# Performance work log

Hardware: AMD Instinct MI355X
Metric: run time of the kernel (lower is better)

## Reference

```python
import jax, jax.numpy as jnp
import numpy as np

NUM_EMBEDDINGS = 1024
EMBEDDING_DIM = 256


def setup_inputs() -> dict:
    key = jax.random.key(0)
    k_in, k_w = jax.random.split(key)
    inputs = jax.random.normal(k_in, (32, EMBEDDING_DIM, 2048), dtype=jnp.float32)
    # nn.Embedding weight initialized uniform in [-1/K, 1/K]
    bound = 1.0 / NUM_EMBEDDINGS
    weight = jax.random.uniform(k_w, (NUM_EMBEDDINGS, EMBEDDING_DIM),
                                dtype=jnp.float32, minval=-bound, maxval=bound)
    return {"inputs": inputs, "weight": weight}


def reference(inputs, weight):
    B, D, T = inputs.shape
    # [B, D, T] -> [B*T, D]
    flat = jnp.transpose(inputs, (0, 2, 1)).reshape(-1, D)
    distances = (jnp.sum(flat * flat, axis=1, keepdims=True)
                 + jnp.sum(weight * weight, axis=1)
                 - 2.0 * flat @ weight.T)  # [N, K]
    encoding_indices = jnp.argmin(distances, axis=1)  # [N]
    # one-hot @ weight is just a gather
    quantized = weight[encoding_indices].reshape(B, T, D)  # [B, T, D]
    quantized = jnp.transpose(quantized, (0, 2, 1))  # [B, D, T]
    # straight-through estimator
    quantized = inputs + jax.lax.stop_gradient(quantized - inputs)
    return quantized, encoding_indices[:, None]
```

## Files before the change

### kernel.cpp

```cpp
#include <hip/hip_runtime.h>


#define VQ_B   32
#define VQ_D   256
#define VQ_T   2048
#define VQ_K   1024

typedef _Float16 f16x8 __attribute__((ext_vector_type(8)));
typedef _Float16 f16x4 __attribute__((ext_vector_type(4)));
typedef float    f32x4 __attribute__((ext_vector_type(4)));

__global__ __launch_bounds__(256) void vq_wprep_kernel(
    const float* __restrict__ w, float* __restrict__ wnorm,
    _Float16* __restrict__ Wh, _Float16* __restrict__ Wl)
{
    __shared__ double ws_[16][16];
    const int tid = threadIdx.x;
    const int kk  = tid >> 4;
    const int dg  = tid & 15;
    const int k   = blockIdx.x * 16 + kk;
    const float* src = w + (size_t)k * VQ_D + dg * 16;
    double s = 0.0;
    #pragma unroll
    for (int q = 0; q < 4; ++q) {
        float4 v = *(const float4*)(src + q * 4);
        s += (double)v.x * v.x + (double)v.y * v.y
           + (double)v.z * v.z + (double)v.w * v.w;
        const float e4[4] = {v.x, v.y, v.z, v.w};
        f16x4 hv, lv;
        #pragma unroll
        for (int j = 0; j < 4; ++j) {
            const float es = e4[j] * 1024.0f;
            const _Float16 h = (_Float16)es;
            hv[j] = h;
            lv[j] = (_Float16)((es - (float)h) * 16777216.0f);
        }
        *(f16x4*)(Wh + (size_t)k * VQ_D + dg * 16 + q * 4) = hv;
        *(f16x4*)(Wl + (size_t)k * VQ_D + dg * 16 + q * 4) = lv;
    }
    ws_[kk][dg] = s;
    __syncthreads();
    if (dg == 0) {
        double acc = 0.0;
        #pragma unroll
        for (int g = 0; g < 16; ++g) acc += ws_[kk][g];
        wnorm[k] = (float)acc;
    }
}

__global__ __launch_bounds__(256, 2) void vq_mfma_kernel(
    const _Float16* __restrict__ Wh, const _Float16* __restrict__ Wl,
    const float* __restrict__ inp,
    const float* __restrict__ wnorm,
    const float* __restrict__ w,
    float* __restrict__ outq, float* __restrict__ outi)
{
    __shared__ alignas(16) char lds[81920];
    char* Xh = lds;
    char* Xl = lds + 32768;
    char* Wb = lds + 65536;

    const int tid  = threadIdx.x;
    const int lane = tid & 63;
    const int wv   = tid >> 6;
    const int m16  = lane & 15;
    const int quad = lane >> 4;
    const int wm   = wv & 1;
    const int wn   = wv >> 1;
    const int b    = blockIdx.x >> 5;
    const int tt0  = (blockIdx.x & 31) * 64;
    const long bt  = (long)b * VQ_T + tt0;

    const int sel  = tid >> 7;
    const int r128 = tid & 127;
    const _Float16* wsrc = (sel ? Wl : Wh) + (size_t)r128 * VQ_D;
    char* wdst = Wb + (sel * 8 + (r128 >> 6) * 4 + ((r128 >> 4) & 3)) * 1024
               + (r128 & 15) * 16;

    f16x8 wreg[4];
    #pragma unroll
    for (int q = 0; q < 4; ++q)
        wreg[q] = *(const f16x8*)(wsrc + q * 8);

    const int xt = m16 + wv * 16;
    double xacc = 0.0;
    {
        float xv[2][8];
        const float* xp0 = inp + ((size_t)b * VQ_D + quad * 8) * VQ_T + tt0 + xt;
        #pragma unroll
        for (int j = 0; j < 8; ++j)
            xv[0][j] = xp0[(size_t)j * VQ_T];
        #pragma unroll
        for (int c = 0; c < 8; ++c) {
            if (c < 7) {
                const float* xpn = inp
                    + ((size_t)b * VQ_D + (c + 1) * 32 + quad * 8) * VQ_T
                    + tt0 + xt;
                #pragma unroll
                for (int j = 0; j < 8; ++j)
                    xv[(c + 1) & 1][j] = xpn[(size_t)j * VQ_T];
            }
            f16x8 hv, lv;
            #pragma unroll
            for (int j = 0; j < 8; ++j) {
                const float x = xv[c & 1][j];
                xacc += (double)x * (double)x;
                const _Float16 h = (_Float16)x;
                hv[j] = h;
                lv[j] = (_Float16)((x - (float)h) * 16777216.0f);
            }
            const int off = ((c * 4 + quad) * 64 + xt) * 16;
            *(f16x8*)(Xh + off) = hv;
            *(f16x8*)(Xl + off) = lv;
        }
    }
    xacc += __shfl_xor(xacc, 16, 64);
    xacc += __shfl_xor(xacc, 32, 64);
    {
        float* xns = (float*)Wb;
        if (quad == 0) xns[xt] = (float)xacc;
    }
    __syncthreads();
    float xnr[2];
    #pragma unroll
    for (int f = 0; f < 2; ++f)
        xnr[f] = ((const float*)Wb)[wn * 32 + f * 16 + m16];
    __syncthreads();

    float bestv[2] = {3.0e38f, 3.0e38f};
    int   besti[2] = {0, 0};
    f32x4 acch[4][2], accl[4][2];

    for (int s = 0; s < 64; ++s) {
        const int c = s & 7;
        #pragma unroll
        for (int q = 0; q < 4; ++q)
            *(f16x8*)(wdst + q * 256) = wreg[q];
        __syncthreads();
        if (s < 63) {
            const int s1  = s + 1;
            const _Float16* src = wsrc
                + (size_t)((s1 >> 3) * 128) * VQ_D + (s1 & 7) * 32;
            #pragma unroll
            for (int q = 0; q < 4; ++q)
                wreg[q] = *(const f16x8*)(src + q * 8);
        }

        if (c == 0) {
            #pragma unroll
            for (int fm = 0; fm < 4; ++fm)
                #pragma unroll
                for (int fn = 0; fn < 2; ++fn) {
                    acch[fm][fn] = (f32x4){0.f, 0.f, 0.f, 0.f};
                    accl[fm][fn] = (f32x4){0.f, 0.f, 0.f, 0.f};
                }
        }

        f16x8 ah[4], al[4], bh[2], bl[2];
        #pragma unroll
        for (int fm = 0; fm < 4; ++fm) {
            ah[fm] = *(const f16x8*)(Wb + (wm * 4 + fm) * 1024 + lane * 16);
            al[fm] = *(const f16x8*)(Wb + (8 + wm * 4 + fm) * 1024 + lane * 16);
        }
        #pragma unroll
        for (int f = 0; f < 2; ++f) {
            const int off = ((c * 4 + quad) * 64 + wn * 32 + f * 16 + m16) * 16;
            bh[f] = *(const f16x8*)(Xh + off);
            bl[f] = *(const f16x8*)(Xl + off);
        }
        #pragma unroll
        for (int fm = 0; fm < 4; ++fm)
            #pragma unroll
            for (int fn = 0; fn < 2; ++fn) {
                acch[fm][fn] = __builtin_amdgcn_mfma_f32_16x16x32_f16(
                    ah[fm], bh[fn], acch[fm][fn], 0, 0, 0);
                accl[fm][fn] = __builtin_amdgcn_mfma_f32_16x16x32_f16(
                    ah[fm], bl[fn], accl[fm][fn], 0, 0, 0);
                accl[fm][fn] = __builtin_amdgcn_mfma_f32_16x16x32_f16(
                    al[fm], bh[fn], accl[fm][fn], 0, 0, 0);
            }

        if (c == 7) {
            const int k0 = (s >> 3) * 128;
            #pragma unroll
            for (int fm = 0; fm < 4; ++fm) {
                #pragma unroll
                for (int r = 0; r < 4; ++r) {
                    const int kg = k0 + wm * 64 + fm * 16 + quad * 4 + r;
                    const float wnk = wnorm[kg];
                    #pragma unroll
                    for (int fn = 0; fn < 2; ++fn) {
                        const float t1 = xnr[fn] + wnk;
                        const float d2 = (acch[fm][fn][r]
                                          + accl[fm][fn][r] * 5.9604644775390625e-8f)
                                         * 0.001953125f;
                        const float sc = t1 - d2;
                        if (sc < bestv[fn]) { bestv[fn] = sc; besti[fn] = kg; }
                    }
                }
            }
        }
        __syncthreads();
    }

    float rv[2]; int ri[2];
    #pragma unroll
    for (int fn = 0; fn < 2; ++fn) {
        float bv = bestv[fn]; int bi = besti[fn];
        #pragma unroll
        for (int mask = 16; mask <= 32; mask <<= 1) {
            const float ov = __shfl_xor(bv, mask, 64);
            const int   oi = __shfl_xor(bi, mask, 64);
            if (ov < bv || (ov == bv && oi < bi)) { bv = ov; bi = oi; }
        }
        rv[fn] = bv; ri[fn] = bi;
    }

    float* sv = (float*)lds;
    int*   si = (int*)(lds + 1024);
    if (quad == 0) {
        #pragma unroll
        for (int fn = 0; fn < 2; ++fn) {
            const int tl = wn * 32 + fn * 16 + m16;
            sv[wm * 64 + tl] = rv[fn];
            si[wm * 64 + tl] = ri[fn];
        }
    }
    __syncthreads();
    if (tid < 64) {
        const float v0 = sv[tid], v1 = sv[64 + tid];
        const int   i0 = si[tid], i1 = si[64 + tid];
        const int   bi = (v1 < v0 || (v1 == v0 && i1 < i0)) ? i1 : i0;
        si[tid] = bi;
        outi[bt + tid] = (float)bi;
    }
    __syncthreads();

    {
        const int t  = tid & 63;
        const int dq = tid >> 6;
        const int bi = si[t];
        const float* wrow = w + (size_t)bi * VQ_D + dq * 64;
        float* obase = outq + ((size_t)b * VQ_D + (size_t)dq * 64) * VQ_T + tt0 + t;
        #pragma unroll 4
        for (int dd = 0; dd < 64; dd += 4) {
            float4 v = *(const float4*)(wrow + dd);
            obase[(size_t)(dd + 0) * VQ_T] = v.x;
            obase[(size_t)(dd + 1) * VQ_T] = v.y;
            obase[(size_t)(dd + 2) * VQ_T] = v.z;
            obase[(size_t)(dd + 3) * VQ_T] = v.w;
        }
    }
}

extern "C" void kernel_launch(void* const* d_in, const int* in_sizes, int n_in,
                              void* d_out, int out_size, void* d_ws, size_t ws_size,
                              hipStream_t stream) {
    const float* inp = (const float*)d_in[0];
    const float* w   = (const float*)d_in[1];
    float* outq  = (float*)d_out;
    float* outi  = outq + (size_t)VQ_B * VQ_D * VQ_T;

    float*    wnorm = (float*)d_ws;
    _Float16* Wh    = (_Float16*)(wnorm + VQ_K);
    _Float16* Wl    = Wh + (size_t)VQ_K * VQ_D;

    vq_wprep_kernel<<<dim3(VQ_K / 16), dim3(256), 0, stream>>>(w, wnorm, Wh, Wl);
    vq_mfma_kernel<<<dim3(VQ_B * (VQ_T / 64)), dim3(256), 0, stream>>>(
        Wh, Wl, inp, wnorm, w, outq, outi);
}
```

Baseline: 247.1 us.

## Stream codebook tiles via global_load_lds double buffer and keep X-high in registers

The codebook tiles are now loaded straight from global memory into LDS with global_load_lds into a double buffer, replacing the register-staged copy. This removes one of the two barriers per step and overlaps the next tile's load with the current MFMAs. The high half of the X fragments is held in registers for the whole loop, which frees LDS and cuts the block's shared memory from 80 KB to 64 KB. The cost is more register pressure from the 16 extra f16x8 values, and the LDS layout has to line up with the lane order of global_load_lds.

```diff
diff --git a/kernel.cpp b/kernel.cpp
--- a/kernel.cpp
+++ b/kernel.cpp
@@ -9,6 +9,10 @@
 typedef _Float16 f16x8 __attribute__((ext_vector_type(8)));
 typedef _Float16 f16x4 __attribute__((ext_vector_type(4)));
 typedef float    f32x4 __attribute__((ext_vector_type(4)));
+
+#define GLOAD_LDS16(gaddr, laddr) \
+  __builtin_amdgcn_global_load_lds((const __attribute__((address_space(1))) void*)(gaddr), \
+                                   (__attribute__((address_space(3))) void*)(laddr), 16, 0, 0)
 
 __global__ __launch_bounds__(256) void vq_wprep_kernel(
     const float* __restrict__ w, float* __restrict__ wnorm,
@@ -55,10 +59,10 @@
     const float* __restrict__ w,
     float* __restrict__ outq, float* __restrict__ outi)
 {
-    __shared__ alignas(16) char lds[81920];
-    char* Xh = lds;
-    char* Xl = lds + 32768;
-    char* Wb = lds + 65536;
+    __shared__ alignas(16) char lds[65536];
+    __shared__ float xns[64];
+    char* Xl  = lds;
+    char* Xhs = lds + 32768;
 
     const int tid  = threadIdx.x;
     const int lane = tid & 63;
@@ -71,17 +75,6 @@
     const int tt0  = (blockIdx.x & 31) * 64;
     const long bt  = (long)b * VQ_T + tt0;
 
-    const int sel  = tid >> 7;
-    const int r128 = tid & 127;
-    const _Float16* wsrc = (sel ? Wl : Wh) + (size_t)r128 * VQ_D;
-    char* wdst = Wb + (sel * 8 + (r128 >> 6) * 4 + ((r128 >> 4) & 3)) * 1024
-               + (r128 & 15) * 16;
-
-    f16x8 wreg[4];
-    #pragma unroll
-    for (int q = 0; q < 4; ++q)
-        wreg[q] = *(const f16x8*)(wsrc + q * 8);
-
     const int xt = m16 + wv * 16;
     double xacc = 0.0;
     {
@@ -110,97 +103,112 @@
                 lv[j] = (_Float16)((x - (float)h) * 16777216.0f);
             }
             const int off = ((c * 4 + quad) * 64 + xt) * 16;
-            *(f16x8*)(Xh + off) = hv;
-            *(f16x8*)(Xl + off) = lv;
+            *(f16x8*)(Xhs + off) = hv;
+            *(f16x8*)(Xl  + off) = lv;
         }
     }
     xacc += __shfl_xor(xacc, 16, 64);
     xacc += __shfl_xor(xacc, 32, 64);
-    {
-        float* xns = (float*)Wb;
-        if (quad == 0) xns[xt] = (float)xacc;
-    }
-    __syncthreads();
+    if (quad == 0) xns[xt] = (float)xacc;
+    __syncthreads();
+
+    f16x8 bhr[8][2];
+    #pragma unroll
+    for (int c = 0; c < 8; ++c)
+        #pragma unroll
+        for (int f = 0; f < 2; ++f)
+            bhr[c][f] = *(const f16x8*)(Xhs +
+                ((c * 4 + quad) * 64 + wn * 32 + f * 16 + m16) * 16);
     float xnr[2];
     #pragma unroll
     for (int f = 0; f < 2; ++f)
-        xnr[f] = ((const float*)Wb)[wn * 32 + f * 16 + m16];
-    __syncthreads();
+        xnr[f] = xns[wn * 32 + f * 16 + m16];
+    __syncthreads();
+
+    const char* gbase = (const char*)((wv >> 1) ? Wl : Wh);
+    const char* gp[4];
+    #pragma unroll
+    for (int i = 0; i < 4; ++i)
+        gp[i] = gbase + (size_t)((wv & 1) * 64 + i * 16 + m16) * 512 + quad * 16;
+
+    #pragma unroll
+    for (int i = 0; i < 4; ++i)
+        GLOAD_LDS16(gp[i], Xhs + (wv * 4 + i) * 1024);
+    #pragma unroll
+    for (int i = 0; i < 4; ++i) gp[i] += 64;
 
     float bestv[2] = {3.0e38f, 3.0e38f};
     int   besti[2] = {0, 0};
     f32x4 acch[4][2], accl[4][2];
 
-    for (int s = 0; s < 64; ++s) {
-        const int c = s & 7;
-        #pragma unroll
-        for (int q = 0; q < 4; ++q)
-            *(f16x8*)(wdst + q * 256) = wreg[q];
-        __syncthreads();
-        if (s < 63) {
-            const int s1  = s + 1;
-            const _Float16* src = wsrc
-                + (size_t)((s1 >> 3) * 128) * VQ_D + (s1 & 7) * 32;
-            #pragma unroll
-            for (int q = 0; q < 4; ++q)
-                wreg[q] = *(const f16x8*)(src + q * 8);
-        }
-
-        if (c == 0) {
-            #pragma unroll
-            for (int fm = 0; fm < 4; ++fm)
-                #pragma unroll
-                for (int fn = 0; fn < 2; ++fn) {
-                    acch[fm][fn] = (f32x4){0.f, 0.f, 0.f, 0.f};
-                    accl[fm][fn] = (f32x4){0.f, 0.f, 0.f, 0.f};
-                }
-        }
-
-        f16x8 ah[4], al[4], bh[2], bl[2];
-        #pragma unroll
-        for (int fm = 0; fm < 4; ++fm) {
-            ah[fm] = *(const f16x8*)(Wb + (wm * 4 + fm) * 1024 + lane * 16);
-            al[fm] = *(const f16x8*)(Wb + (8 + wm * 4 + fm) * 1024 + lane * 16);
-        }
-        #pragma unroll
-        for (int f = 0; f < 2; ++f) {
-            const int off = ((c * 4 + quad) * 64 + wn * 32 + f * 16 + m16) * 16;
-            bh[f] = *(const f16x8*)(Xh + off);
-            bl[f] = *(const f16x8*)(Xl + off);
-        }
-        #pragma unroll
-        for (int fm = 0; fm < 4; ++fm)
-            #pragma unroll
-            for (int fn = 0; fn < 2; ++fn) {
-                acch[fm][fn] = __builtin_amdgcn_mfma_f32_16x16x32_f16(
-                    ah[fm], bh[fn], acch[fm][fn], 0, 0, 0);
-                accl[fm][fn] = __builtin_amdgcn_mfma_f32_16x16x32_f16(
-                    ah[fm], bl[fn], accl[fm][fn], 0, 0, 0);
-                accl[fm][fn] = __builtin_amdgcn_mfma_f32_16x16x32_f16(
-                    al[fm], bh[fn], accl[fm][fn], 0, 0, 0);
-            }
-
-        if (c == 7) {
-            const int k0 = (s >> 3) * 128;
-            #pragma unroll
-            for (int fm = 0; fm < 4; ++fm) {
-                #pragma unroll
-                for (int r = 0; r < 4; ++r) {
-                    const int kg = k0 + wm * 64 + fm * 16 + quad * 4 + r;
-                    const float wnk = wnorm[kg];
+    for (int g = 0; g < 8; ++g) {
+        #pragma unroll
+        for (int c = 0; c < 8; ++c) {
+            char* const Wcur = Xhs + (c & 1) * 16384;
+            char* const Wnxt = Xhs + ((c & 1) ^ 1) * 16384;
+            __syncthreads();
+            if (g < 7 || c < 7) {
+                #pragma unroll
+                for (int i = 0; i < 4; ++i)
+                    GLOAD_LDS16(gp[i], Wnxt + (wv * 4 + i) * 1024);
+                const long adv = (c == 6) ? (65536L - 448L) : 64L;
+                #pragma unroll
+                for (int i = 0; i < 4; ++i) gp[i] += adv;
+            }
+            if (c == 0) {
+                #pragma unroll
+                for (int fm = 0; fm < 4; ++fm)
                     #pragma unroll
                     for (int fn = 0; fn < 2; ++fn) {
-                        const float t1 = xnr[fn] + wnk;
-                        const float d2 = (acch[fm][fn][r]
-                                          + accl[fm][fn][r] * 5.9604644775390625e-8f)
-                                         * 0.001953125f;
-                        const float sc = t1 - d2;
-                        if (sc < bestv[fn]) { bestv[fn] = sc; besti[fn] = kg; }
+                        acch[fm][fn] = (f32x4){0.f, 0.f, 0.f, 0.f};
+                        accl[fm][fn] = (f32x4){0.f, 0.f, 0.f, 0.f};
+                    }
+            }
+
+            f16x8 ah[4], al[4], bl[2];
+            #pragma unroll
+            for (int fm = 0; fm < 4; ++fm) {
+                ah[fm] = *(const f16x8*)(Wcur + (wm * 4 + fm) * 1024 + lane * 16);
+                al[fm] = *(const f16x8*)(Wcur + (8 + wm * 4 + fm) * 1024 + lane * 16);
+            }
+            #pragma unroll
+            for (int f = 0; f < 2; ++f)
+                bl[f] = *(const f16x8*)(Xl +
+                    ((c * 4 + quad) * 64 + wn * 32 + f * 16 + m16) * 16);
+
+            #pragma unroll
+            for (int fm = 0; fm < 4; ++fm)
+                #pragma unroll
+                for (int fn = 0; fn < 2; ++fn) {
+                    acch[fm][fn] = __builtin_amdgcn_mfma_f32_16x16x32_f16(
+                        ah[fm], bhr[c][fn], acch[fm][fn], 0, 0, 0);
+                    accl[fm][fn] = __builtin_amdgcn_mfma_f32_16x16x32_f16(
+                        ah[fm], bl[fn], accl[fm][fn], 0, 0, 0);
+                    accl[fm][fn] = __builtin_amdgcn_mfma_f32_16x16x32_f16(
+                        al[fm], bhr[c][fn], accl[fm][fn], 0, 0, 0);
+                }
+
+            if (c == 7) {
+                const int k0 = g * 128;
+                #pragma unroll
+                for (int fm = 0; fm < 4; ++fm) {
+                    #pragma unroll
+                    for (int r = 0; r < 4; ++r) {
+                        const int kg = k0 + wm * 64 + fm * 16 + quad * 4 + r;
+                        const float wnk = wnorm[kg];
+                        #pragma unroll
+                        for (int fn = 0; fn < 2; ++fn) {
+                            const float t1 = xnr[fn] + wnk;
+                            const float d2 = (acch[fm][fn][r]
+                                              + accl[fm][fn][r] * 5.9604644775390625e-8f)
+                                             * 0.001953125f;
+                            const float sc = t1 - d2;
+                            if (sc < bestv[fn]) { bestv[fn] = sc; besti[fn] = kg; }
+                        }
                     }
                 }
             }
         }
-        __syncthreads();
     }
 
     float rv[2]; int ri[2];
@@ -216,6 +224,7 @@
         rv[fn] = bv; ri[fn] = bi;
     }
 
+    __syncthreads();
     float* sv = (float*)lds;
     int*   si = (int*)(lds + 1024);
     if (quad == 0) {
```

Measured after the change: 252.7 us. 2.3% more time.

## Stream pre-swizzled codebook fragments from global memory directly into MFMA registers

Applied to the files above, without the earlier changes.

The prep kernel now writes the fp16 hi/lo codebook in an MFMA fragment-ordered layout, so the main kernel loads A operands straight from global/L2 into registers with double-buffered register prefetch. This removes the per-step LDS staging of the codebook and its two block barriers per step. The time tile shrinks to 32 and LDS use drops, allowing 4 blocks per CU with 2048 blocks in total. In exchange, each block reads the full codebook from L2 with less reuse per load, and per-wave MFMA work per step is smaller.

```diff
diff --git a/kernel.cpp b/kernel.cpp
--- a/kernel.cpp
+++ b/kernel.cpp
@@ -12,13 +12,15 @@
 
 __global__ __launch_bounds__(256) void vq_wprep_kernel(
     const float* __restrict__ w, float* __restrict__ wnorm,
-    _Float16* __restrict__ Wh, _Float16* __restrict__ Wl)
+    _Float16* __restrict__ WTh, _Float16* __restrict__ WTl)
 {
     __shared__ double ws_[16][16];
     const int tid = threadIdx.x;
     const int kk  = tid >> 4;
     const int dg  = tid & 15;
     const int k   = blockIdx.x * 16 + kk;
+    const int R   = k >> 4;
+    const int r16 = k & 15;
     const float* src = w + (size_t)k * VQ_D + dg * 16;
     double s = 0.0;
     #pragma unroll
@@ -35,8 +37,11 @@
             hv[j] = h;
             lv[j] = (_Float16)((es - (float)h) * 16777216.0f);
         }
-        *(f16x4*)(Wh + (size_t)k * VQ_D + dg * 16 + q * 4) = hv;
-        *(f16x4*)(Wl + (size_t)k * VQ_D + dg * 16 + q * 4) = lv;
+        const size_t off = (size_t)(((R * 8 + (dg >> 1)) * 64
+                          + ((dg & 1) * 2 + (q >> 1)) * 16 + r16) * 16)
+                          + (q & 1) * 8;
+        *(f16x4*)((char*)WTh + off) = hv;
+        *(f16x4*)((char*)WTl + off) = lv;
     }
     ws_[kk][dg] = s;
     __syncthreads();
@@ -48,159 +53,162 @@
     }
 }
 
-__global__ __launch_bounds__(256, 2) void vq_mfma_kernel(
-    const _Float16* __restrict__ Wh, const _Float16* __restrict__ Wl,
+#define VQ_STEP(CUR_H, CUR_L, NXT_H, NXT_L, CC, LAST)                      \
+  {                                                                        \
+    if (!(LAST)) {                                                         \
+      _Pragma("unroll")                                                    \
+      for (int fm = 0; fm < 2; ++fm) {                                     \
+        NXT_H[fm] = *(const f16x8*)pwh[fm];                                \
+        NXT_L[fm] = *(const f16x8*)pwl[fm];                                \
+      }                                                                    \
+      const long adv_ = ((CC) == 6) ? 58368L : 1024L;                      \
+      pwh[0] += adv_; pwh[1] += adv_; pwl[0] += adv_; pwl[1] += adv_;      \
+    }                                                                      \
+    f16x8 bh_[2], bl_[2];                                                  \
+    _Pragma("unroll")                                                      \
+    for (int fn = 0; fn < 2; ++fn) {                                       \
+      const int xoff_ = (((CC) * 4 + quad) * 32 + fn * 16 + m16) * 16;     \
+      bh_[fn] = *(const f16x8*)(Xh + xoff_);                               \
+      bl_[fn] = *(const f16x8*)(Xl + xoff_);                               \
+    }                                                                      \
+    _Pragma("unroll")                                                      \
+    for (int fm = 0; fm < 2; ++fm)                                         \
+      _Pragma("unroll")                                                    \
+      for (int fn = 0; fn < 2; ++fn) {                                     \
+        acch[fm][fn] = __builtin_amdgcn_mfma_f32_16x16x32_f16(             \
+            CUR_H[fm], bh_[fn], acch[fm][fn], 0, 0, 0);                    \
+        accl[fm][fn] = __builtin_amdgcn_mfma_f32_16x16x32_f16(             \
+            CUR_H[fm], bl_[fn], accl[fm][fn], 0, 0, 0);                    \
+        accl[fm][fn] = __builtin_amdgcn_mfma_f32_16x16x32_f16(             \
+            CUR_L[fm], bh_[fn], accl[fm][fn], 0, 0, 0);                    \
+      }                                                                    \
+  }
+
+__global__ __launch_bounds__(256, 4) void vq_mfma_kernel(
+    const _Float16* __restrict__ WTh, const _Float16* __restrict__ WTl,
     const float* __restrict__ inp,
     const float* __restrict__ wnorm,
     const float* __restrict__ w,
     float* __restrict__ outq, float* __restrict__ outi)
 {
-    __shared__ alignas(16) char lds[81920];
+    __shared__ alignas(16) char lds[32768 + 2048 + 128];
     char* Xh = lds;
-    char* Xl = lds + 32768;
-    char* Wb = lds + 65536;
+    char* Xl = lds + 16384;
+    double* xs  = (double*)(lds + 32768);
+    float*  xns = (float*)(lds + 32768 + 2048);
 
     const int tid  = threadIdx.x;
     const int lane = tid & 63;
     const int wv   = tid >> 6;
     const int m16  = lane & 15;
     const int quad = lane >> 4;
-    const int wm   = wv & 1;
-    const int wn   = wv >> 1;
-    const int b    = blockIdx.x >> 5;
-    const int tt0  = (blockIdx.x & 31) * 64;
+    const int wm   = wv;
+    const int b    = blockIdx.x >> 6;
+    const int tt0  = (blockIdx.x & 63) * 32;
     const long bt  = (long)b * VQ_T + tt0;
 
-    const int sel  = tid >> 7;
-    const int r128 = tid & 127;
-    const _Float16* wsrc = (sel ? Wl : Wh) + (size_t)r128 * VQ_D;
-    char* wdst = Wb + (sel * 8 + (r128 >> 6) * 4 + ((r128 >> 4) & 3)) * 1024
-               + (r128 & 15) * 16;
-
-    f16x8 wreg[4];
-    #pragma unroll
-    for (int q = 0; q < 4; ++q)
-        wreg[q] = *(const f16x8*)(wsrc + q * 8);
-
-    const int xt = m16 + wv * 16;
-    double xacc = 0.0;
     {
-        float xv[2][8];
-        const float* xp0 = inp + ((size_t)b * VQ_D + quad * 8) * VQ_T + tt0 + xt;
-        #pragma unroll
-        for (int j = 0; j < 8; ++j)
-            xv[0][j] = xp0[(size_t)j * VQ_T];
-        #pragma unroll
-        for (int c = 0; c < 8; ++c) {
-            if (c < 7) {
-                const float* xpn = inp
-                    + ((size_t)b * VQ_D + (c + 1) * 32 + quad * 8) * VQ_T
-                    + tt0 + xt;
-                #pragma unroll
-                for (int j = 0; j < 8; ++j)
-                    xv[(c + 1) & 1][j] = xpn[(size_t)j * VQ_T];
-            }
+        const int po = tid >> 5;
+        const int pt = tid & 31;
+        double xacc = 0.0;
+        const float* xp = inp + ((size_t)b * VQ_D + po * 32) * VQ_T + tt0 + pt;
+        #pragma unroll
+        for (int q = 0; q < 4; ++q) {
+            float xv[8];
+            #pragma unroll
+            for (int j = 0; j < 8; ++j)
+                xv[j] = xp[(size_t)(q * 8 + j) * VQ_T];
             f16x8 hv, lv;
             #pragma unroll
             for (int j = 0; j < 8; ++j) {
-                const float x = xv[c & 1][j];
+                const float x = xv[j];
                 xacc += (double)x * (double)x;
                 const _Float16 h = (_Float16)x;
                 hv[j] = h;
                 lv[j] = (_Float16)((x - (float)h) * 16777216.0f);
             }
-            const int off = ((c * 4 + quad) * 64 + xt) * 16;
+            const int off = ((po * 4 + q) * 32 + pt) * 16;
             *(f16x8*)(Xh + off) = hv;
             *(f16x8*)(Xl + off) = lv;
         }
-    }
-    xacc += __shfl_xor(xacc, 16, 64);
-    xacc += __shfl_xor(xacc, 32, 64);
-    {
-        float* xns = (float*)Wb;
-        if (quad == 0) xns[xt] = (float)xacc;
-    }
-    __syncthreads();
+        xs[po * 32 + pt] = xacc;
+    }
+    __syncthreads();
+    if (tid < 32) {
+        double s = xs[tid];
+        #pragma unroll
+        for (int o = 1; o < 8; ++o) s += xs[o * 32 + tid];
+        xns[tid] = (float)s;
+    }
+    __syncthreads();
+
     float xnr[2];
     #pragma unroll
     for (int f = 0; f < 2; ++f)
-        xnr[f] = ((const float*)Wb)[wn * 32 + f * 16 + m16];
-    __syncthreads();
+        xnr[f] = xns[f * 16 + m16];
+
+    const char* pwh[2];
+    const char* pwl[2];
+    #pragma unroll
+    for (int fm = 0; fm < 2; ++fm) {
+        const size_t base = (size_t)(wm * 2 + fm) * 8192 + (size_t)lane * 16;
+        pwh[fm] = (const char*)WTh + base;
+        pwl[fm] = (const char*)WTl + base;
+    }
+    f16x8 aAh[2], aAl[2], aBh[2], aBl[2];
+    #pragma unroll
+    for (int fm = 0; fm < 2; ++fm) {
+        aAh[fm] = *(const f16x8*)pwh[fm];
+        aAl[fm] = *(const f16x8*)pwl[fm];
+    }
+    pwh[0] += 1024; pwh[1] += 1024; pwl[0] += 1024; pwl[1] += 1024;
 
     float bestv[2] = {3.0e38f, 3.0e38f};
     int   besti[2] = {0, 0};
-    f32x4 acch[4][2], accl[4][2];
-
-    for (int s = 0; s < 64; ++s) {
-        const int c = s & 7;
-        #pragma unroll
-        for (int q = 0; q < 4; ++q)
-            *(f16x8*)(wdst + q * 256) = wreg[q];
-        __syncthreads();
-        if (s < 63) {
-            const int s1  = s + 1;
-            const _Float16* src = wsrc
-                + (size_t)((s1 >> 3) * 128) * VQ_D + (s1 & 7) * 32;
-            #pragma unroll
-            for (int q = 0; q < 4; ++q)
-                wreg[q] = *(const f16x8*)(src + q * 8);
-        }
-
-        if (c == 0) {
-            #pragma unroll
-            for (int fm = 0; fm < 4; ++fm)
+    f32x4 acch[2][2], accl[2][2];
+
+    for (int g = 0; g < 8; ++g) {
+        float wnr[2][4];
+        #pragma unroll
+        for (int fm = 0; fm < 2; ++fm)
+            #pragma unroll
+            for (int r = 0; r < 4; ++r)
+                wnr[fm][r] = wnorm[g * 128 + wm * 32 + fm * 16 + quad * 4 + r];
+
+        #pragma unroll
+        for (int fm = 0; fm < 2; ++fm)
+            #pragma unroll
+            for (int fn = 0; fn < 2; ++fn) {
+                acch[fm][fn] = (f32x4){0.f, 0.f, 0.f, 0.f};
+                accl[fm][fn] = (f32x4){0.f, 0.f, 0.f, 0.f};
+            }
+
+        VQ_STEP(aAh, aAl, aBh, aBl, 0, false)
+        VQ_STEP(aBh, aBl, aAh, aAl, 1, false)
+        VQ_STEP(aAh, aAl, aBh, aBl, 2, false)
+        VQ_STEP(aBh, aBl, aAh, aAl, 3, false)
+        VQ_STEP(aAh, aAl, aBh, aBl, 4, false)
+        VQ_STEP(aBh, aBl, aAh, aAl, 5, false)
+        VQ_STEP(aAh, aAl, aBh, aBl, 6, false)
+        VQ_STEP(aBh, aBl, aAh, aAl, 7, (g == 7))
+
+        #pragma unroll
+        for (int fm = 0; fm < 2; ++fm) {
+            #pragma unroll
+            for (int r = 0; r < 4; ++r) {
+                const int kg = g * 128 + wm * 32 + fm * 16 + quad * 4 + r;
+                const float wnk = wnr[fm][r];
                 #pragma unroll
                 for (int fn = 0; fn < 2; ++fn) {
-                    acch[fm][fn] = (f32x4){0.f, 0.f, 0.f, 0.f};
-                    accl[fm][fn] = (f32x4){0.f, 0.f, 0.f, 0.f};
-                }
-        }
-
-        f16x8 ah[4], al[4], bh[2], bl[2];
-        #pragma unroll
-        for (int fm = 0; fm < 4; ++fm) {
-            ah[fm] = *(const f16x8*)(Wb + (wm * 4 + fm) * 1024 + lane * 16);
-            al[fm] = *(const f16x8*)(Wb + (8 + wm * 4 + fm) * 1024 + lane * 16);
-        }
-        #pragma unroll
-        for (int f = 0; f < 2; ++f) {
-            const int off = ((c * 4 + quad) * 64 + wn * 32 + f * 16 + m16) * 16;
-            bh[f] = *(const f16x8*)(Xh + off);
-            bl[f] = *(const f16x8*)(Xl + off);
-        }
-        #pragma unroll
-        for (int fm = 0; fm < 4; ++fm)
-            #pragma unroll
-            for (int fn = 0; fn < 2; ++fn) {
-                acch[fm][fn] = __builtin_amdgcn_mfma_f32_16x16x32_f16(
-                    ah[fm], bh[fn], acch[fm][fn], 0, 0, 0);
-                accl[fm][fn] = __builtin_amdgcn_mfma_f32_16x16x32_f16(
-                    ah[fm], bl[fn], accl[fm][fn], 0, 0, 0);
-                accl[fm][fn] = __builtin_amdgcn_mfma_f32_16x16x32_f16(
-                    al[fm], bh[fn], accl[fm][fn], 0, 0, 0);
-            }
-
-        if (c == 7) {
-            const int k0 = (s >> 3) * 128;
-            #pragma unroll
-            for (int fm = 0; fm < 4; ++fm) {
-                #pragma unroll
-                for (int r = 0; r < 4; ++r) {
-                    const int kg = k0 + wm * 64 + fm * 16 + quad * 4 + r;
-                    const float wnk = wnorm[kg];
-                    #pragma unroll
-                    for (int fn = 0; fn < 2; ++fn) {
-                        const float t1 = xnr[fn] + wnk;
-                        const float d2 = (acch[fm][fn][r]
-                                          + accl[fm][fn][r] * 5.9604644775390625e-8f)
-                                         * 0.001953125f;
-                        const float sc = t1 - d2;
-                        if (sc < bestv[fn]) { bestv[fn] = sc; besti[fn] = kg; }
-                    }
+                    const float t1 = xnr[fn] + wnk;
+                    const float d2 = (acch[fm][fn][r]
+                                      + accl[fm][fn][r] * 5.9604644775390625e-8f)
+                                     * 0.001953125f;
+                    const float sc = t1 - d2;
+                    if (sc < bestv[fn]) { bestv[fn] = sc; besti[fn] = kg; }
                 }
             }
         }
-        __syncthreads();
     }
 
     float rv[2]; int ri[2];
@@ -216,34 +224,40 @@
         rv[fn] = bv; ri[fn] = bi;
     }
 
-    float* sv = (float*)lds;
-    int*   si = (int*)(lds + 1024);
+    __syncthreads();
+    float* sv  = (float*)lds;
+    int*   si_ = (int*)(lds + 512);
+    int*   sif = (int*)(lds + 1536);
     if (quad == 0) {
         #pragma unroll
         for (int fn = 0; fn < 2; ++fn) {
-            const int tl = wn * 32 + fn * 16 + m16;
-            sv[wm * 64 + tl] = rv[fn];
-            si[wm * 64 + tl] = ri[fn];
-        }
-    }
-    __syncthreads();
-    if (tid < 64) {
-        const float v0 = sv[tid], v1 = sv[64 + tid];
-        const int   i0 = si[tid], i1 = si[64 + tid];
-        const int   bi = (v1 < v0 || (v1 == v0 && i1 < i0)) ? i1 : i0;
-        si[tid] = bi;
+            const int tl = fn * 16 + m16;
+            sv[wm * 32 + tl] = rv[fn];
+            si_[wm * 32 + tl] = ri[fn];
+        }
+    }
+    __syncthreads();
+    if (tid < 32) {
+        float bv = sv[tid]; int bi = si_[tid];
+        #pragma unroll
+        for (int wq = 1; wq < 4; ++wq) {
+            const float v = sv[wq * 32 + tid];
+            const int   i = si_[wq * 32 + tid];
+            if (v < bv || (v == bv && i < bi)) { bv = v; bi = i; }
+        }
+        sif[tid] = bi;
         outi[bt + tid] = (float)bi;
     }
     __syncthreads();
 
     {
-        const int t  = tid & 63;
-        const int dq = tid >> 6;
-        const int bi = si[t];
-        const float* wrow = w + (size_t)bi * VQ_D + dq * 64;
-        float* obase = outq + ((size_t)b * VQ_D + (size_t)dq * 64) * VQ_T + tt0 + t;
+        const int t  = tid & 31;
+        const int dg = tid >> 5;
+        const int bi = sif[t];
+        const float* wrow = w + (size_t)bi * VQ_D + dg * 32;
+        float* obase = outq + ((size_t)b * VQ_D + (size_t)dg * 32) * VQ_T + tt0 + t;
         #pragma unroll 4
-        for (int dd = 0; dd < 64; dd += 4) {
+        for (int dd = 0; dd < 32; dd += 4) {
             float4 v = *(const float4*)(wrow + dd);
             obase[(size_t)(dd + 0) * VQ_T] = v.x;
             obase[(size_t)(dd + 1) * VQ_T] = v.y;
@@ -262,10 +276,10 @@
     float* outi  = outq + (size_t)VQ_B * VQ_D * VQ_T;
 
     float*    wnorm = (float*)d_ws;
-    _Float16* Wh    = (_Float16*)(wnorm + VQ_K);
-    _Float16* Wl    = Wh + (size_t)VQ_K * VQ_D;
-
-    vq_wprep_kernel<<<dim3(VQ_K / 16), dim3(256), 0, stream>>>(w, wnorm, Wh, Wl);
-    vq_mfma_kernel<<<dim3(VQ_B * (VQ_T / 64)), dim3(256), 0, stream>>>(
-        Wh, Wl, inp, wnorm, w, outq, outi);
+    _Float16* WTh   = (_Float16*)(wnorm + VQ_K);
+    _Float16* WTl   = WTh + (size_t)VQ_K * VQ_D;
+
+    vq_wprep_kernel<<<dim3(VQ_K / 16), dim3(256), 0, stream>>>(w, wnorm, WTh, WTl);
+    vq_mfma_kernel<<<dim3(VQ_B * (VQ_T / 32)), dim3(256), 0, stream>>>(
+        WTh, WTl, inp, wnorm, w, outq, outi);
 }
```

Result: slower. 480.9 us (+94.6%).
